# Optimization experiments

Measured on AMD Instinct MI355X. Metric: run time of the kernel, lower is better.

## Reference

```python
import jax, jax.numpy as jnp
import numpy as np

N_NODES = 100000
N_EDGES = 1600000
NODE_DIM = 128
EDGE_DIM = 32
HIDDEN_DIM = 256


def _linear_params(key, fan_in, fan_out):
    kw, kb = jax.random.split(key)
    bound = 1.0 / np.sqrt(fan_in)
    W = jax.random.uniform(kw, (fan_in, fan_out), minval=-bound, maxval=bound, dtype=jnp.float32)
    b = jax.random.uniform(kb, (fan_out,), minval=-bound, maxval=bound, dtype=jnp.float32)
    return W, b


def setup_inputs() -> dict:
    key = jax.random.key(0)
    ks = jax.random.split(key, 8)
    x = jax.random.normal(ks[0], (N_NODES, NODE_DIM), dtype=jnp.float32)
    edge_index = jax.random.randint(ks[1], (2, N_EDGES), 0, N_NODES, dtype=jnp.int64)
    edge_attr = jax.random.normal(ks[2], (N_EDGES, EDGE_DIM), dtype=jnp.float32)
    congestion = jax.random.uniform(ks[3], (N_NODES,), dtype=jnp.float32)
    msg_in = 2 * NODE_DIM + EDGE_DIM + 1
    mW1, mb1 = _linear_params(ks[4], msg_in, HIDDEN_DIM)
    mW2, mb2 = _linear_params(ks[5], HIDDEN_DIM, NODE_DIM)
    uW1, ub1 = _linear_params(ks[6], 2 * NODE_DIM, HIDDEN_DIM)
    uW2, ub2 = _linear_params(ks[7], HIDDEN_DIM, NODE_DIM)
    return {
        "x": x, "edge_index": edge_index, "edge_attr": edge_attr, "congestion": congestion,
        "mW1": mW1, "mb1": mb1, "mW2": mW2, "mb2": mb2,
        "uW1": uW1, "ub1": ub1, "uW2": uW2, "ub2": ub2,
    }


def reference(x, edge_index, edge_attr, congestion, mW1, mb1, mW2, mb2, uW1, ub1, uW2, ub2):
    src, dst = edge_index[0], edge_index[1]
    # gather node features and src congestion, concat along feature dim  [E, 2D+edge_dim+1]
    msg_in = jnp.concatenate(
        [x[src], x[dst], edge_attr, congestion[src][:, None]], axis=-1)
    h = jax.nn.relu(msg_in @ mW1 + mb1)          # [E, hidden]
    messages = h @ mW2 + mb2                     # [E, node_dim]
    # scatter_add messages into destination nodes  [N, node_dim]
    aggregated = jax.ops.segment_sum(messages, dst, num_segments=x.shape[0])
    upd_in = jnp.concatenate([x, aggregated], axis=-1)  # [N, 2*node_dim]
    h2 = jax.nn.relu(upd_in @ uW1 + ub1)
    x_new = h2 @ uW2 + ub2                       # [N, node_dim]
    return x_new
```

## Files before the change

kernel.cpp:

```cpp
#include <hip/hip_runtime.h>

#define E_TOTAL 1600000
#define NN 100000
#define D 128
#define ED 32
#define H 256

typedef __attribute__((ext_vector_type(8))) short s16x8;
typedef __attribute__((ext_vector_type(4))) short s16x4;
typedef __attribute__((ext_vector_type(4))) float f32x4;

#define MFMA(a, b, c) __builtin_amdgcn_mfma_f32_16x16x32_bf16((a), (b), (c), 0, 0, 0)

__device__ __forceinline__ short f2bf(float f) {
    unsigned u = __builtin_bit_cast(unsigned, f);
    u += 0x7fffu + ((u >> 16) & 1u);
    return (short)(u >> 16);
}
__device__ __forceinline__ float bf2f(short s) {
    return __builtin_bit_cast(float, ((unsigned)(unsigned short)s) << 16);
}

__device__ __forceinline__ void gll16(const void* g, void* l) {
    __builtin_amdgcn_global_load_lds(
        (const __attribute__((address_space(1))) void*)g,
        (__attribute__((address_space(3))) void*)l, 16, 0, 0);
}

__device__ __forceinline__ void swz_one(const float* __restrict__ W,
                                        short* __restrict__ out,
                                        int K, int N, int idx) {
    int j    = idx & 7;
    int lane = (idx >> 3) & 63;
    int rest = idx >> 9;
    int NT   = N >> 4;
    int nt   = rest % NT;
    int t    = rest / NT;
    int k    = t * 32 + (lane >> 4) * 8 + j;
    int col  = nt * 16 + (lane & 15);
    out[idx] = f2bf((k < K) ? W[k * N + col] : 0.f);
}

__global__ void k_prep(const float* __restrict__ x, short* __restrict__ xb,
                       const int* __restrict__ ei, int* __restrict__ cnt,
                       const float* __restrict__ mW1, short* __restrict__ W1s,
                       const float* __restrict__ mW2, short* __restrict__ W2s,
                       const float* __restrict__ uW1, short* __restrict__ U1s,
                       const float* __restrict__ uW2, short* __restrict__ U2s) {
    const int b = blockIdx.x;
    if (b < 12500) {
        int i = (b * 256 + threadIdx.x) * 4;
        if (i >= NN * D) return;
        f32x4 v = *(const f32x4*)(x + i);
        s16x4 o;
        o[0] = f2bf(v[0]); o[1] = f2bf(v[1]); o[2] = f2bf(v[2]); o[3] = f2bf(v[3]);
        *(s16x4*)(xb + i) = o;
    } else if (b < 18750) {
        int e = (b - 12500) * 256 + threadIdx.x;
        if (e < E_TOTAL) atomicAdd(&cnt[ei[E_TOTAL + e]], 1);
    } else {
        int idx = (b - 18750) * 256 + threadIdx.x;
        if (idx < 81920) { swz_one(mW1, W1s, 289, 256, idx); return; }
        idx -= 81920;
        if (idx < 32768) { swz_one(mW2, W2s, 256, 128, idx); return; }
        idx -= 32768;
        if (idx < 65536) { swz_one(uW1, U1s, 256, 256, idx); return; }
        idx -= 65536;
        if (idx < 32768) { swz_one(uW2, U2s, 256, 128, idx); }
    }
}

__global__ void k_scanc(int* __restrict__ cnt, unsigned long long* __restrict__ chain,
                        int n) {
    __shared__ int wsum[16];
    __shared__ int woff[16];
    __shared__ int carry_s;
    const int tid = threadIdx.x, lane = tid & 63, wv = tid >> 6;
    int i = blockIdx.x * 1024 + tid;
    int v = (i < n) ? cnt[i] : 0;
    int s = v;
#pragma unroll
    for (int off = 1; off < 64; off <<= 1) {
        int u = __shfl_up(s, off, 64);
        if (lane >= off) s += u;
    }
    if (lane == 63) wsum[wv] = s;
    __syncthreads();
    if (wv == 0 && lane < 16) {
        int t = wsum[lane];
        int sc = t;
#pragma unroll
        for (int off = 1; off < 16; off <<= 1) {
            int u = __shfl_up(sc, off, 16);
            if (lane >= off) sc += u;
        }
        woff[lane] = sc - t;
    }
    __syncthreads();
    int excl = (s - v) + woff[wv];
    if (tid == 1023) {
        int btot = excl + v;
        __hip_atomic_store(&chain[blockIdx.x], (1ull << 32) | (unsigned)btot,
                           __ATOMIC_RELAXED, __HIP_MEMORY_SCOPE_AGENT);
        int pfx = 0;
        for (int j = (int)blockIdx.x - 1; j >= 0; --j) {
            unsigned long long e;
            do {
                e = __hip_atomic_load(&chain[j], __ATOMIC_RELAXED,
                                      __HIP_MEMORY_SCOPE_AGENT);
            } while ((e >> 32) == 0);
            pfx += (int)(unsigned)e;
            if ((e >> 32) == 2) break;
        }
        __hip_atomic_store(&chain[blockIdx.x], (2ull << 32) | (unsigned)(pfx + btot),
                           __ATOMIC_RELAXED, __HIP_MEMORY_SCOPE_AGENT);
        carry_s = pfx;
    }
    __syncthreads();
    if (i < n) cnt[i] = excl + carry_s;
}

__global__ void k_agginit(const int* __restrict__ cnt, const float* __restrict__ b2,
                          float* __restrict__ agg) {
    int i4 = (blockIdx.x * 256 + threadIdx.x) * 4;
    if (i4 >= NN * D) return;
    int node  = i4 >> 7;
    int c     = i4 & 127;
    int start = cnt[node];
    int end   = (node < NN - 1) ? cnt[node + 1] : E_TOTAL;
    float deg = (float)(end - start);
    f32x4 bv = *(const f32x4*)(b2 + c);
    f32x4 o;
#pragma unroll
    for (int j = 0; j < 4; j++) o[j] = deg * bv[j];
    *(f32x4*)(agg + i4) = o;
}

__global__ void k_perm(const int* __restrict__ ei, int* __restrict__ cursor,
                       int* __restrict__ perm, int2* __restrict__ srcdst) {
    int e = blockIdx.x * blockDim.x + threadIdx.x;
    if (e >= E_TOTAL) return;
    int s = ei[e], d = ei[E_TOTAL + e];
    int pos = atomicAdd(&cursor[d], 1);
    perm[pos] = e;
    srcdst[pos] = make_int2(s, d);
}

__global__ __launch_bounds__(512, 4)
void k_pre(const short* __restrict__ xb, const short* __restrict__ W1s,
           const float* __restrict__ b1, short* __restrict__ ys,
           short* __restrict__ yd) {
    __shared__ char smem[32768];
    const int tid  = threadIdx.x;
    const int lane = tid & 63;
    const int w    = tid >> 6;
    const int eh   = w >> 2;
    const int cg   = w & 3;
    const int m    = lane & 15;
    const int q    = lane >> 4;
    const int r0   = blockIdx.x * 128;

    {
        int rowl = w * 16 + (lane >> 2);
        int grow = r0 + rowl;
        int gc   = grow < NN ? grow : 0;
        int kqs  = (lane & 3) ^ ((lane >> 3) & 3);
        const char* gx = (const char*)xb + (long)gc * 256 + kqs * 16;
#pragma unroll
        for (int t = 0; t < 4; t++)
            gll16(gx + t * 64, smem + t * 8192 + w * 1024);
    }
    __syncthreads();

    const int rdoff = m * 64 + ((q ^ ((m >> 1) & 3)) << 4);

    float b1c[4];
#pragma unroll
    for (int n = 0; n < 4; n++) b1c[n] = b1[cg * 64 + n * 16 + m];

#pragma unroll
    for (int pass = 0; pass < 2; pass++) {
        f32x4 acc[4][4];
#pragma unroll
        for (int mt = 0; mt < 4; mt++)
#pragma unroll
            for (int n = 0; n < 4; n++) acc[mt][n] = (f32x4){0.f, 0.f, 0.f, 0.f};
#pragma unroll
        for (int t = 0; t < 4; t++) {
            s16x8 b[4];
            const short* bw = W1s + ((pass * 4 + t) * 16 + cg * 4) * 512 + lane * 8;
#pragma unroll
            for (int n = 0; n < 4; n++) b[n] = *(const s16x8*)(bw + n * 512);
#pragma unroll
            for (int mt = 0; mt < 4; mt++) {
                s16x8 a = *(const s16x8*)(smem + t * 8192 + (eh * 4 + mt) * 1024 + rdoff);
#pragma unroll
                for (int n = 0; n < 4; n++) acc[mt][n] = MFMA(a, b[n], acc[mt][n]);
            }
        }
        short* out = pass ? yd : ys;
#pragma unroll
        for (int mt = 0; mt < 4; mt++)
#pragma unroll
            for (int r = 0; r < 4; r++) {
                int grow = r0 + eh * 64 + mt * 16 + q * 4 + r;
                if (grow < NN) {
                    s16x4 o;
#pragma unroll
                    for (int n = 0; n < 4; n++)
                        o[n] = f2bf(acc[mt][n][r] + (pass ? 0.f : b1c[n]));
                    *(s16x4*)(out + (long)grow * 256 + (cg * 16 + m) * 4) = o;
                }
            }
    }
}

__global__ __launch_bounds__(512, 4)
void k_edge(const int* __restrict__ perm, const int2* __restrict__ srcdst,
            const short* __restrict__ ys, const short* __restrict__ yd,
            const float* __restrict__ eattr, const float* __restrict__ cong,
            const short* __restrict__ W1s, const short* __restrict__ W2s,
            float* __restrict__ agg) {
    __shared__ char smem[73728];
    __shared__ int   dst_s[128];
    __shared__ int   src_s[128];
    __shared__ short cong_s[128];

    const int tid  = threadIdx.x;
    const int lane = tid & 63;
    const int w    = tid >> 6;
    const int eh   = w >> 2;
    const int cg   = w & 3;
    const int m    = lane & 15;
    const int q    = lane >> 4;
    const int p0b  = blockIdx.x * 128;

    {
        int edge = w * 16 + (lane >> 2);
        int kqs  = (lane & 3) ^ ((lane >> 3) & 3);
        int ea = perm[p0b + edge];
        const float* ge = eattr + (long)ea * ED + kqs * 8;
        f32x4 e0 = *(const f32x4*)ge, e1 = *(const f32x4*)(ge + 4);
        s16x8 ev;
#pragma unroll
        for (int j = 0; j < 4; j++) { ev[j] = f2bf(e0[j]); ev[4 + j] = f2bf(e1[j]); }
        *(s16x8*)(smem + w * 1024 + lane * 16) = ev;
        if (tid < 128) {
            int2 sd2 = srcdst[p0b + tid];
            dst_s[tid]  = sd2.y;
            src_s[tid]  = sd2.x;
            cong_s[tid] = f2bf(cong[sd2.x]);
        }
    }
    __syncthreads();

    const int rdoff = m * 64 + ((q ^ ((m >> 1) & 3)) << 4);

    f32x4 acc[4][4];
#pragma unroll
    for (int mt = 0; mt < 4; mt++)
#pragma unroll
        for (int n = 0; n < 4; n++) acc[mt][n] = (f32x4){0.f, 0.f, 0.f, 0.f};

    {
        s16x8 b[4];
        const short* bw = W1s + (8 * 16 + cg * 4) * 512 + lane * 8;
#pragma unroll
        for (int n = 0; n < 4; n++) b[n] = *(const s16x8*)(bw + n * 512);
#pragma unroll
        for (int mt = 0; mt < 4; mt++) {
            s16x8 a = *(const s16x8*)(smem + (eh * 4 + mt) * 1024 + rdoff);
#pragma unroll
            for (int n = 0; n < 4; n++) acc[mt][n] = MFMA(a, b[n], acc[mt][n]);
        }
    }
    {
        s16x8 b[4];
        const short* bw = W1s + (9 * 16 + cg * 4) * 512 + lane * 8;
#pragma unroll
        for (int n = 0; n < 4; n++) b[n] = *(const s16x8*)(bw + n * 512);
#pragma unroll
        for (int mt = 0; mt < 4; mt++) {
            s16x8 a = (s16x8){0, 0, 0, 0, 0, 0, 0, 0};
            short cv = cong_s[eh * 64 + mt * 16 + m];
            a[0] = (q == 0) ? cv : (short)0;
#pragma unroll
            for (int n = 0; n < 4; n++) acc[mt][n] = MFMA(a, b[n], acc[mt][n]);
        }
    }

    {
        short* hb16 = (short*)(smem + 8192);
        const int qoff = (cg * 16 + m) * 4;
#pragma unroll
        for (int mt = 0; mt < 4; mt++) {
            s16x4 ysv[4], ydv[4];
#pragma unroll
            for (int r = 0; r < 4; r++) {
                int e = eh * 64 + mt * 16 + q * 4 + r;
                ysv[r] = *(const s16x4*)(ys + (long)src_s[e] * 256 + qoff);
                ydv[r] = *(const s16x4*)(yd + (long)dst_s[e] * 256 + qoff);
            }
#pragma unroll
            for (int r = 0; r < 4; r++) {
                int e = eh * 64 + mt * 16 + q * 4 + r;
                int key = (2 * q + (r >> 1)) & 3;
#pragma unroll
                for (int n = 0; n < 4; n++) {
                    const int chunk = 2 * cg + (n >> 1);
                    const int srq   = (n & 1) * 2 + (m >> 3);
                    int phys = srq ^ key;
                    float v = acc[mt][n][r] + bf2f(ysv[r][n]) + bf2f(ydv[r][n]);
                    hb16[chunk * 4096 + e * 32 + phys * 8 + (m & 7)] =
                        f2bf(v > 0.f ? v : 0.f);
                }
            }
        }
    }
    __syncthreads();

    f32x4 acc2[4][2];
#pragma unroll
    for (int mt = 0; mt < 4; mt++) {
        acc2[mt][0] = (f32x4){0.f, 0.f, 0.f, 0.f};
        acc2[mt][1] = (f32x4){0.f, 0.f, 0.f, 0.f};
    }
#pragma unroll
    for (int t2 = 0; t2 < 8; t2++) {
        const short* bw = W2s + (t2 * 8 + cg * 2) * 512 + lane * 8;
        s16x8 b0  = *(const s16x8*)bw;
        s16x8 b1v = *(const s16x8*)(bw + 512);
#pragma unroll
        for (int mt = 0; mt < 4; mt++) {
            s16x8 a = *(const s16x8*)(smem + 8192 + t2 * 8192
                                      + (eh * 4 + mt) * 1024 + rdoff);
            acc2[mt][0] = MFMA(a, b0, acc2[mt][0]);
            acc2[mt][1] = MFMA(a, b1v, acc2[mt][1]);
        }
    }
    __syncthreads();

    {
        float (*mbuf)[132] = (float (*)[132])smem;
#pragma unroll
        for (int mt = 0; mt < 4; mt++)
#pragma unroll
            for (int r = 0; r < 4; r++) {
                int edge = eh * 64 + mt * 16 + q * 4 + r;
                mbuf[edge][cg * 32 + m]      = acc2[mt][0][r];
                mbuf[edge][cg * 32 + 16 + m] = acc2[mt][1][r];
            }
    }
    __syncthreads();

    {
        float (*mbuf)[132] = (float (*)[132])smem;
        const int qtr = tid >> 7, cc = tid & 127;
        float s = 0.f;
        int prev = dst_s[qtr * 32];
        for (int row = qtr * 32; row < qtr * 32 + 32; row++) {
            int dcur = dst_s[row];
            if (dcur != prev) {
                __hip_atomic_fetch_add(agg + (long)prev * D + cc, s,
                                       __ATOMIC_RELAXED, __HIP_MEMORY_SCOPE_AGENT);
                s = 0.f; prev = dcur;
            }
            s += mbuf[row][cc];
        }
        __hip_atomic_fetch_add(agg + (long)prev * D + cc, s,
                               __ATOMIC_RELAXED, __HIP_MEMORY_SCOPE_AGENT);
    }
}

__global__ __launch_bounds__(512, 4)
void k_node(const short* __restrict__ xb, const float* __restrict__ agg,
            const short* __restrict__ U1s, const float* __restrict__ b1,
            const short* __restrict__ U2s, const float* __restrict__ b2,
            float* __restrict__ out) {
    __shared__ char smem[65536];
    const int tid  = threadIdx.x;
    const int lane = tid & 63;
    const int w    = tid >> 6;
    const int eh   = w >> 2;
    const int cg   = w & 3;
    const int m    = lane & 15;
    const int q    = lane >> 4;
    const int r0   = blockIdx.x * 128;

    {
        int rowl = w * 16 + (lane >> 2);
        int grow = r0 + rowl;
        int gc   = grow < NN ? grow : 0;
        int kqs  = (lane & 3) ^ ((lane >> 3) & 3);
        const char* gx = (const char*)xb + (long)gc * 256 + kqs * 16;
#pragma unroll
        for (int t = 0; t < 4; t++)
            gll16(gx + t * 64, smem + t * 8192 + w * 1024);
        const float* ga = agg + (long)gc * D + kqs * 8;
#pragma unroll
        for (int t = 0; t < 4; t++) {
            f32x4 a0 = *(const f32x4*)(ga + t * 32);
            f32x4 a1 = *(const f32x4*)(ga + t * 32 + 4);
            s16x8 v;
#pragma unroll
            for (int j = 0; j < 4; j++) { v[j] = f2bf(a0[j]); v[4 + j] = f2bf(a1[j]); }
            *(s16x8*)(smem + (4 + t) * 8192 + w * 1024 + lane * 16) = v;
        }
    }
    __syncthreads();

    const int rdoff = m * 64 + ((q ^ ((m >> 1) & 3)) << 4);

    f32x4 acc[4][4];
#pragma unroll
    for (int mt = 0; mt < 4; mt++)
#pragma unroll
        for (int n = 0; n < 4; n++) acc[mt][n] = (f32x4){0.f, 0.f, 0.f, 0.f};

#pragma unroll
    for (int t = 0; t < 8; t++) {
        s16x8 b[4];
        const short* bw = U1s + (t * 16 + cg * 4) * 512 + lane * 8;
#pragma unroll
        for (int n = 0; n < 4; n++) b[n] = *(const s16x8*)(bw + n * 512);
#pragma unroll
        for (int mt = 0; mt < 4; mt++) {
            s16x8 a = *(const s16x8*)(smem + t * 8192 + (eh * 4 + mt) * 1024 + rdoff);
#pragma unroll
            for (int n = 0; n < 4; n++) acc[mt][n] = MFMA(a, b[n], acc[mt][n]);
        }
    }
    __syncthreads();

    {
        short* hb16 = (short*)smem;
#pragma unroll
        for (int n = 0; n < 4; n++) {
            const int chunk = 2 * cg + (n >> 1);
            const int srq   = (n & 1) * 2 + (m >> 3);
            const float bias = b1[cg * 64 + n * 16 + m];
#pragma unroll
            for (int mt = 0; mt < 4; mt++) {
#pragma unroll
                for (int r = 0; r < 4; r++) {
                    int row = eh * 64 + mt * 16 + q * 4 + r;
                    int key = (2 * q + (r >> 1)) & 3;
                    int phys = srq ^ key;
                    float v = acc[mt][n][r] + bias;
                    hb16[chunk * 4096 + row * 32 + phys * 8 + (m & 7)] =
                        f2bf(v > 0.f ? v : 0.f);
                }
            }
        }
    }
    __syncthreads();

    f32x4 acc2[4][2];
#pragma unroll
    for (int mt = 0; mt < 4; mt++) {
        acc2[mt][0] = (f32x4){0.f, 0.f, 0.f, 0.f};
        acc2[mt][1] = (f32x4){0.f, 0.f, 0.f, 0.f};
    }
#pragma unroll
    for (int t2 = 0; t2 < 8; t2++) {
        const short* bw = U2s + (t2 * 8 + cg * 2) * 512 + lane * 8;
        s16x8 b0  = *(const s16x8*)bw;
        s16x8 b1v = *(const s16x8*)(bw + 512);
#pragma unroll
        for (int mt = 0; mt < 4; mt++) {
            s16x8 a = *(const s16x8*)(smem + t2 * 8192 + (eh * 4 + mt) * 1024 + rdoff);
            acc2[mt][0] = MFMA(a, b0, acc2[mt][0]);
            acc2[mt][1] = MFMA(a, b1v, acc2[mt][1]);
        }
    }

    {
        float bb0 = b2[cg * 32 + m];
        float bb1 = b2[cg * 32 + 16 + m];
#pragma unroll
        for (int mt = 0; mt < 4; mt++)
#pragma unroll
            for (int r = 0; r < 4; r++) {
                int grow = r0 + eh * 64 + mt * 16 + q * 4 + r;
                if (grow < NN) {
                    out[(long)grow * D + cg * 32 + m]      = acc2[mt][0][r] + bb0;
                    out[(long)grow * D + cg * 32 + 16 + m] = acc2[mt][1][r] + bb1;
                }
            }
    }
}

extern "C" void kernel_launch(void* const* d_in, const int* in_sizes, int n_in,
                              void* d_out, int out_size, void* d_ws, size_t ws_size,
                              hipStream_t stream) {
    const float* x     = (const float*)d_in[0];
    const int*   ei    = (const int*)d_in[1];
    const float* eattr = (const float*)d_in[2];
    const float* cong  = (const float*)d_in[3];
    const float* mW1   = (const float*)d_in[4];
    const float* mb1   = (const float*)d_in[5];
    const float* mW2   = (const float*)d_in[6];
    const float* mb2   = (const float*)d_in[7];
    const float* uW1   = (const float*)d_in[8];
    const float* ub1   = (const float*)d_in[9];
    const float* uW2   = (const float*)d_in[10];
    const float* ub2   = (const float*)d_in[11];

    char* ws = (char*)d_ws;
    float* agg    = (float*)ws;
    short* xb     = (short*)(ws + 51200000);
    short* W1s    = (short*)(ws + 76800000);
    short* W2s    = (short*)(ws + 76963840);
    short* U1s    = (short*)(ws + 77029376);
    short* U2s    = (short*)(ws + 77160448);
    int*   cnt    = (int*)(ws + 77225984);
    unsigned long long* chain = (unsigned long long*)(ws + 77625984);
    int*   perm   = (int*)(ws + 77627008);
    int2*  srcdst = (int2*)(ws + 84027008);
    short* yd     = (short*)(ws + 96827008);
    short* ys     = (short*)(ws + 148027008);

    hipMemsetAsync(cnt, 0, 401024, stream);

    k_prep<<<19582, 256, 0, stream>>>(x, xb, ei, cnt,
                                      mW1, W1s, mW2, W2s, uW1, U1s, uW2, U2s);

    k_pre<<<(NN + 127) / 128, 512, 0, stream>>>(xb, W1s, mb1, ys, yd);

    int nb = (NN + 1023) / 1024;
    k_scanc<<<nb, 1024, 0, stream>>>(cnt, chain, NN);

    k_agginit<<<12500, 256, 0, stream>>>(cnt, mb2, agg);

    k_perm<<<(E_TOTAL + 255) / 256, 256, 0, stream>>>(ei, cnt, perm, srcdst);

    k_edge<<<E_TOTAL / 128, 512, 0, stream>>>(perm, srcdst, ys, yd, eattr, cong,
                                              W1s, W2s, agg);
    k_node<<<(NN + 127) / 128, 512, 0, stream>>>(xb, agg, U1s, ub1, U2s, ub2,
                                                 (float*)d_out);
}
```

Before: 922.3 us.

## Use row-major XOR-swizzled hidden tile with vectorized stores; fuse agg init into scan

The hidden activation tile in shared memory for the edge and node kernels becomes row-major and XOR-swizzled. Each lane now writes four bf16 values as one 8-byte store instead of scalar 2-byte stores, and the second-layer weights are pre-permuted along K to match the new column order. The aggregate-buffer initialisation (degree times bias) moves into the scan kernel using degrees held in shared memory, which removes one launch and the re-read of the prefix array. The risks are wrong results if the K permutation does not exactly match the swizzled layout, and extra work in the scan kernel, which runs on few blocks.

```diff
diff --git a/kernel.cpp b/kernel.cpp
--- a/kernel.cpp
+++ b/kernel.cpp
@@ -39,6 +39,20 @@
     int k    = t * 32 + (lane >> 4) * 8 + j;
     int col  = nt * 16 + (lane & 15);
     out[idx] = f2bf((k < K) ? W[k * N + col] : 0.f);
+}
+
+__device__ __forceinline__ void swz_kp(const float* __restrict__ W,
+                                       short* __restrict__ out, int N, int idx) {
+    int j    = idx & 7;
+    int lane = (idx >> 3) & 63;
+    int rest = idx >> 9;
+    int NT   = N >> 4;
+    int nt   = rest % NT;
+    int t    = rest / NT;
+    int p    = t * 32 + (lane >> 4) * 8 + j;
+    int k    = (p >> 6) * 64 + (p & 3) * 16 + ((p >> 2) & 15);
+    int col  = nt * 16 + (lane & 15);
+    out[idx] = f2bf(W[k * N + col]);
 }
 
 __global__ void k_prep(const float* __restrict__ x, short* __restrict__ xb,
@@ -62,19 +76,21 @@
         int idx = (b - 18750) * 256 + threadIdx.x;
         if (idx < 81920) { swz_one(mW1, W1s, 289, 256, idx); return; }
         idx -= 81920;
-        if (idx < 32768) { swz_one(mW2, W2s, 256, 128, idx); return; }
+        if (idx < 32768) { swz_kp(mW2, W2s, 128, idx); return; }
         idx -= 32768;
         if (idx < 65536) { swz_one(uW1, U1s, 256, 256, idx); return; }
         idx -= 65536;
-        if (idx < 32768) { swz_one(uW2, U2s, 256, 128, idx); }
+        if (idx < 32768) { swz_kp(uW2, U2s, 128, idx); }
     }
 }
 
 __global__ void k_scanc(int* __restrict__ cnt, unsigned long long* __restrict__ chain,
+                        const float* __restrict__ b2, float* __restrict__ agg,
                         int n) {
     __shared__ int wsum[16];
     __shared__ int woff[16];
     __shared__ int carry_s;
+    __shared__ int deg_s[1024];
     const int tid = threadIdx.x, lane = tid & 63, wv = tid >> 6;
     int i = blockIdx.x * 1024 + tid;
     int v = (i < n) ? cnt[i] : 0;
@@ -116,24 +132,25 @@
                            __ATOMIC_RELAXED, __HIP_MEMORY_SCOPE_AGENT);
         carry_s = pfx;
     }
+    deg_s[tid] = v;
     __syncthreads();
     if (i < n) cnt[i] = excl + carry_s;
-}
-
-__global__ void k_agginit(const int* __restrict__ cnt, const float* __restrict__ b2,
-                          float* __restrict__ agg) {
-    int i4 = (blockIdx.x * 256 + threadIdx.x) * 4;
-    if (i4 >= NN * D) return;
-    int node  = i4 >> 7;
-    int c     = i4 & 127;
-    int start = cnt[node];
-    int end   = (node < NN - 1) ? cnt[node + 1] : E_TOTAL;
-    float deg = (float)(end - start);
-    f32x4 bv = *(const f32x4*)(b2 + c);
-    f32x4 o;
-#pragma unroll
-    for (int j = 0; j < 4; j++) o[j] = deg * bv[j];
-    *(f32x4*)(agg + i4) = o;
+
+    const int base = blockIdx.x * 1024;
+#pragma unroll
+    for (int it = 0; it < 32; it++) {
+        int idx  = it * 1024 + tid;
+        int node = base + (idx >> 5);
+        if (node < n) {
+            float deg = (float)deg_s[idx >> 5];
+            int c = (idx & 31) * 4;
+            f32x4 bv = *(const f32x4*)(b2 + c);
+            f32x4 o;
+#pragma unroll
+            for (int j = 0; j < 4; j++) o[j] = deg * bv[j];
+            *(f32x4*)(agg + (long)node * D + c) = o;
+        }
+    }
 }
 
 __global__ void k_perm(const int* __restrict__ ei, int* __restrict__ cursor,
@@ -290,8 +307,10 @@
     }
 
     {
-        short* hb16 = (short*)(smem + 8192);
+        char* hbase = smem + 8192;
         const int qoff = (cg * 16 + m) * 4;
+        const int s0   = (cg * 16 + m) >> 1;
+        const int half = (m & 1) * 8;
 #pragma unroll
         for (int mt = 0; mt < 4; mt++) {
             s16x4 ysv[4], ydv[4];
@@ -304,16 +323,14 @@
 #pragma unroll
             for (int r = 0; r < 4; r++) {
                 int e = eh * 64 + mt * 16 + q * 4 + r;
-                int key = (2 * q + (r >> 1)) & 3;
+                int sl = s0 ^ (e & 31);
+                s16x4 o;
 #pragma unroll
                 for (int n = 0; n < 4; n++) {
-                    const int chunk = 2 * cg + (n >> 1);
-                    const int srq   = (n & 1) * 2 + (m >> 3);
-                    int phys = srq ^ key;
                     float v = acc[mt][n][r] + bf2f(ysv[r][n]) + bf2f(ydv[r][n]);
-                    hb16[chunk * 4096 + e * 32 + phys * 8 + (m & 7)] =
-                        f2bf(v > 0.f ? v : 0.f);
+                    o[n] = f2bf(v > 0.f ? v : 0.f);
                 }
+                *(s16x4*)(hbase + e * 512 + sl * 16 + half) = o;
             }
         }
     }
@@ -332,8 +349,9 @@
         s16x8 b1v = *(const s16x8*)(bw + 512);
 #pragma unroll
         for (int mt = 0; mt < 4; mt++) {
-            s16x8 a = *(const s16x8*)(smem + 8192 + t2 * 8192
-                                      + (eh * 4 + mt) * 1024 + rdoff);
+            int e  = eh * 64 + mt * 16 + m;
+            int sl = (t2 * 4 + q) ^ (e & 31);
+            s16x8 a = *(const s16x8*)(smem + 8192 + e * 512 + sl * 16);
             acc2[mt][0] = MFMA(a, b0, acc2[mt][0]);
             acc2[mt][1] = MFMA(a, b1v, acc2[mt][1]);
         }
@@ -433,23 +451,25 @@
     __syncthreads();
 
     {
-        short* hb16 = (short*)smem;
-#pragma unroll
-        for (int n = 0; n < 4; n++) {
-            const int chunk = 2 * cg + (n >> 1);
-            const int srq   = (n & 1) * 2 + (m >> 3);
-            const float bias = b1[cg * 64 + n * 16 + m];
-#pragma unroll
-            for (int mt = 0; mt < 4; mt++) {
-#pragma unroll
-                for (int r = 0; r < 4; r++) {
-                    int row = eh * 64 + mt * 16 + q * 4 + r;
-                    int key = (2 * q + (r >> 1)) & 3;
-                    int phys = srq ^ key;
-                    float v = acc[mt][n][r] + bias;
-                    hb16[chunk * 4096 + row * 32 + phys * 8 + (m & 7)] =
-                        f2bf(v > 0.f ? v : 0.f);
+        char* hbase = smem;
+        const int s0   = (cg * 16 + m) >> 1;
+        const int half = (m & 1) * 8;
+        float b1c[4];
+#pragma unroll
+        for (int n = 0; n < 4; n++) b1c[n] = b1[cg * 64 + n * 16 + m];
+#pragma unroll
+        for (int mt = 0; mt < 4; mt++) {
+#pragma unroll
+            for (int r = 0; r < 4; r++) {
+                int row = eh * 64 + mt * 16 + q * 4 + r;
+                int sl  = s0 ^ (row & 31);
+                s16x4 o;
+#pragma unroll
+                for (int n = 0; n < 4; n++) {
+                    float v = acc[mt][n][r] + b1c[n];
+                    o[n] = f2bf(v > 0.f ? v : 0.f);
                 }
+                *(s16x4*)(hbase + row * 512 + sl * 16 + half) = o;
             }
         }
     }
@@ -468,7 +488,9 @@
         s16x8 b1v = *(const s16x8*)(bw + 512);
 #pragma unroll
         for (int mt = 0; mt < 4; mt++) {
-            s16x8 a = *(const s16x8*)(smem + t2 * 8192 + (eh * 4 + mt) * 1024 + rdoff);
+            int row = eh * 64 + mt * 16 + m;
+            int sl  = (t2 * 4 + q) ^ (row & 31);
+            s16x8 a = *(const s16x8*)(smem + row * 512 + sl * 16);
             acc2[mt][0] = MFMA(a, b0, acc2[mt][0]);
             acc2[mt][1] = MFMA(a, b1v, acc2[mt][1]);
         }
@@ -528,9 +550,7 @@
     k_pre<<<(NN + 127) / 128, 512, 0, stream>>>(xb, W1s, mb1, ys, yd);
 
     int nb = (NN + 1023) / 1024;
-    k_scanc<<<nb, 1024, 0, stream>>>(cnt, chain, NN);
-
-    k_agginit<<<12500, 256, 0, stream>>>(cnt, mb2, agg);
+    k_scanc<<<nb, 1024, 0, stream>>>(cnt, chain, mb2, agg, NN);
 
     k_perm<<<(E_TOTAL + 255) / 256, 256, 0, stream>>>(ei, cnt, perm, srcdst);
 
```

New measurement: 932.2 us. No clear change (+1.1%).
